# Optimization experiments

Hardware: AMD Instinct MI355X
Metric: run time of the kernel (lower is better)

Reference implementation:

```python
import jax, jax.numpy as jnp
import numpy as np

INPUT, HIDDEN = 128, 64
B, T = 512, 1024


def _lstm_dir(x, Wih, Whh, b):
    """Single-direction LSTM (PyTorch gate order i,f,g,o). x: [B,T,I] -> [B,T,H]."""
    Bn = x.shape[0]
    H = Whh.shape[1]
    # precompute input contributions for all timesteps: [B,T,4H]
    xg = jnp.einsum('bti,gi->btg', x, Wih) + b

    def step(carry, g_t):
        h, c = carry
        g = g_t + h @ Whh.T  # [B,4H]
        i, f, gg, o = jnp.split(g, 4, axis=-1)
        c = jax.nn.sigmoid(f) * c + jax.nn.sigmoid(i) * jnp.tanh(gg)
        h = jax.nn.sigmoid(o) * jnp.tanh(c)
        return (h, c), h

    h0 = jnp.zeros((Bn, H), x.dtype)
    (_, _), hs = jax.lax.scan(step, (h0, h0), jnp.swapaxes(xg, 0, 1))
    return jnp.swapaxes(hs, 0, 1)  # [B,T,H]


def setup_inputs() -> dict:
    key = jax.random.key(0)
    ks = jax.random.split(key, 9)
    s_ih = 1.0 / np.sqrt(HIDDEN)
    def u(k, shape):
        return jax.random.uniform(k, shape, jnp.float32, -s_ih, s_ih)
    return {
        'x': jax.random.normal(ks[0], (B, T, INPUT), jnp.float32),
        'Wih_f': u(ks[1], (4 * HIDDEN, INPUT)),
        'Whh_f': u(ks[2], (4 * HIDDEN, HIDDEN)),
        'b_f': u(ks[3], (4 * HIDDEN,)),   # b_ih + b_hh folded (same math)
        'Wih_b': u(ks[4], (4 * HIDDEN, INPUT)),
        'Whh_b': u(ks[5], (4 * HIDDEN, HIDDEN)),
        'b_b': u(ks[6], (4 * HIDDEN,)),
    }


def reference(x, Wih_f, Whh_f, b_f, Wih_b, Whh_b, b_b):
    # forward returns the full bidirectional sequence output [B,T,2H]
    out_f = _lstm_dir(x, Wih_f, Whh_f, b_f)
    out_b = _lstm_dir(x[:, ::-1], Wih_b, Whh_b, b_b)[:, ::-1]
    return jnp.concatenate([out_f, out_b], axis=-1)
```

## Files before the change

### kernel.cpp

```cpp
#include <hip/hip_runtime.h>

#define T_LEN 1024
#define IN_DIM 128
#define HID 64
#define XSTR 160
#define HSTR 96

typedef __attribute__((ext_vector_type(8))) short short8;
typedef __attribute__((ext_vector_type(4))) float floatx4;
typedef __attribute__((ext_vector_type(2))) float floatx2;

__device__ __forceinline__ unsigned short f2bf(float v) {
    union { float f; unsigned u; } a; a.f = v;
    unsigned r = a.u + 0x7FFFu + ((a.u >> 16) & 1u);
    return (unsigned short)(r >> 16);
}

__device__ __forceinline__ short8 cvt8(const float* p) {
    short8 r;
#pragma unroll
    for (int j = 0; j < 8; ++j) r[j] = (short)f2bf(p[j]);
    return r;
}

#define LOG2E 1.44269504088896f
__device__ __forceinline__ float sigm(float x) {
    return __builtin_amdgcn_rcpf(1.0f + __builtin_amdgcn_exp2f(x * -LOG2E));
}
__device__ __forceinline__ float tanh_(float x) {
    return 2.0f * __builtin_amdgcn_rcpf(1.0f + __builtin_amdgcn_exp2f(x * -2.0f * LOG2E)) - 1.0f;
}


__global__ __launch_bounds__(256, 1) void lstm_bidir(
    const float* __restrict__ x,
    const float* __restrict__ WihF, const float* __restrict__ WhhF, const float* __restrict__ bF,
    const float* __restrict__ WihB, const float* __restrict__ WhhB, const float* __restrict__ bB,
    float* __restrict__ out)
{
    const int tid  = threadIdx.x;
    const int w    = tid >> 6;
    const int lane = tid & 63;
    const int nloc = lane & 15;
    const int quad = lane >> 4;
    const int bid  = blockIdx.x;
    const int dir  = bid & 1;
    const int b0   = (bid >> 1) * 4;

    const float* Wih  = dir ? WihB : WihF;
    const float* Whh  = dir ? WhhB : WhhF;
    const float* bias = dir ? bB   : bF;

    __shared__ unsigned short x_s[2][4 * XSTR];
    __shared__ unsigned short h_s[2][4 * HSTR];

    for (int i = tid; i < 2 * 4 * HSTR; i += 256) ((unsigned short*)h_s)[i] = 0;

    short8 wihf[4][4];
    short8 whhf[4][2];
    float  bv[4];
#pragma unroll
    for (int gc = 0; gc < 4; ++gc) {
        const int row = gc * 64 + w * 16 + nloc;
        bv[gc] = bias[row];
#pragma unroll
        for (int kf = 0; kf < 4; ++kf)
            wihf[gc][kf] = cvt8(Wih + row * IN_DIM + kf * 32 + quad * 8);
#pragma unroll
        for (int kf = 0; kf < 2; ++kf)
            whhf[gc][kf] = cvt8(Whh + row * HID + kf * 32 + quad * 8);
    }

    const int sr = tid >> 6;
    const int sk = (tid & 63) * 2;
    const float* xrow = x + (size_t)(b0 + sr) * T_LEN * IN_DIM + sk;

    auto tmap = [&](int s) {
        int ss = s < T_LEN - 1 ? s : T_LEN - 1;
        return dir ? (T_LEN - 1 - ss) : ss;
    };

    auto stage = [&](int s, int buf) {
        floatx2 v = *(const floatx2*)(xrow + (size_t)tmap(s) * IN_DIM);
        unsigned pack = (unsigned)f2bf(v.x) | ((unsigned)f2bf(v.y) << 16);
        *(unsigned*)&x_s[buf][sr * XSTR + sk] = pack;
    };
    stage(0, 0);
    stage(1, 1);
    floatx2 pfA = *(const floatx2*)(xrow + (size_t)tmap(2) * IN_DIM);
    floatx2 pfB = *(const floatx2*)(xrow + (size_t)tmap(3) * IN_DIM);

    float c = 0.f;

    __syncthreads();

    floatx4 xacc0[4], xacc1[4];
    {
        short8 xa[4];
        const unsigned short* xb = &x_s[0][(nloc >> 2) * XSTR + quad * 8];
#pragma unroll
        for (int kf = 0; kf < 4; ++kf) xa[kf] = *(const short8*)(xb + kf * 32);
        __syncthreads();
#pragma unroll
        for (int gc = 0; gc < 4; ++gc) xacc0[gc] = (floatx4){bv[gc], bv[gc], bv[gc], bv[gc]};
#pragma unroll
        for (int kf = 0; kf < 4; ++kf)
#pragma unroll
            for (int gc = 0; gc < 4; ++gc)
                xacc0[gc] = __builtin_amdgcn_mfma_f32_16x16x32_bf16(xa[kf], wihf[gc][kf], xacc0[gc], 0, 0, 0);
    }

    float* outcol = out + ((size_t)(b0 + quad) * T_LEN) * 128 + dir * HID + w * 16 + nloc;

    auto step = [&](int t, int cur, floatx4* xaccC, floatx4* xaccN, floatx2& pf) {
        floatx2 old = pf;
        pf = *(const floatx2*)(xrow + (size_t)tmap(t + 4) * IN_DIM);

        short8 ha[2];
        const unsigned short* hb = &h_s[cur][(nloc >> 2) * HSTR + quad * 8];
#pragma unroll
        for (int kf = 0; kf < 2; ++kf) ha[kf] = *(const short8*)(hb + kf * 32);

        short8 xa[4];
        const unsigned short* xb = &x_s[cur ^ 1][(nloc >> 2) * XSTR + quad * 8];
#pragma unroll
        for (int kf = 0; kf < 4; ++kf) xa[kf] = *(const short8*)(xb + kf * 32);

        floatx4 acc[4];
#pragma unroll
        for (int gc = 0; gc < 4; ++gc)
            acc[gc] = __builtin_amdgcn_mfma_f32_16x16x32_bf16(ha[0], whhf[gc][0], xaccC[gc], 0, 0, 0);
#pragma unroll
        for (int gc = 0; gc < 4; ++gc)
            acc[gc] = __builtin_amdgcn_mfma_f32_16x16x32_bf16(ha[1], whhf[gc][1], acc[gc], 0, 0, 0);

#pragma unroll
        for (int gc = 0; gc < 4; ++gc) xaccN[gc] = (floatx4){bv[gc], bv[gc], bv[gc], bv[gc]};
#pragma unroll
        for (int kf = 0; kf < 4; ++kf)
#pragma unroll
            for (int gc = 0; gc < 4; ++gc)
                xaccN[gc] = __builtin_amdgcn_mfma_f32_16x16x32_bf16(xa[kf], wihf[gc][kf], xaccN[gc], 0, 0, 0);

        const int tg = tmap(t);
        {
            float iv = sigm(acc[0][0]);
            float fv = sigm(acc[1][0]);
            float gv = tanh_(acc[2][0]);
            float ov = sigm(acc[3][0]);
            c = fv * c + iv * gv;
            float hv = ov * tanh_(c);
            outcol[(size_t)tg * 128] = hv;
            h_s[cur ^ 1][quad * HSTR + w * 16 + nloc] = f2bf(hv);
        }
        {
            unsigned pack = (unsigned)f2bf(old.x) | ((unsigned)f2bf(old.y) << 16);
            *(unsigned*)&x_s[cur][sr * XSTR + sk] = pack;
        }
        __syncthreads();
    };

    for (int t = 0; t < T_LEN; t += 2) {
        step(t,     0, xacc0, xacc1, pfA);
        step(t + 1, 1, xacc1, xacc0, pfB);
    }
}

extern "C" void kernel_launch(void* const* d_in, const int* in_sizes, int n_in,
                              void* d_out, int out_size, void* d_ws, size_t ws_size,
                              hipStream_t stream) {
    const float* x    = (const float*)d_in[0];
    const float* WihF = (const float*)d_in[1];
    const float* WhhF = (const float*)d_in[2];
    const float* bF   = (const float*)d_in[3];
    const float* WihB = (const float*)d_in[4];
    const float* WhhB = (const float*)d_in[5];
    const float* bB   = (const float*)d_in[6];
    float* out = (float*)d_out;

    lstm_bidir<<<dim3(256), dim3(256), 0, stream>>>(x, WihF, WhhF, bF, WihB, WhhB, bB, out);
}
```

Measured before the change: 835.6 us.

## Stage x and output in 8-step chunks through shared memory with vector I/O

Replaces per-timestep scalar x prefetch and scalar output stores with chunked staging: 8 timesteps of x are loaded as float4 per thread one chunk ahead into double-buffered LDS, and h outputs are buffered in LDS and flushed as coalesced float4 stores one chunk later. The aim is to cut global memory transaction count and latency exposure on the serial recurrence path. It adds LDS usage and makes some steps heavier than others (load/convert on the first two steps of each chunk), which can lengthen those iterations.

```diff
diff --git a/kernel.cpp b/kernel.cpp
--- a/kernel.cpp
+++ b/kernel.cpp
@@ -3,12 +3,15 @@
 #define T_LEN 1024
 #define IN_DIM 128
 #define HID 64
+#define CH 8
+#define NCH (T_LEN / CH)
 #define XSTR 160
 #define HSTR 96
+#define OSTR 72
 
 typedef __attribute__((ext_vector_type(8))) short short8;
 typedef __attribute__((ext_vector_type(4))) float floatx4;
-typedef __attribute__((ext_vector_type(2))) float floatx2;
+typedef __attribute__((ext_vector_type(2))) unsigned uintx2;
 
 __device__ __forceinline__ unsigned short f2bf(float v) {
     union { float f; unsigned u; } a; a.f = v;
@@ -30,7 +33,6 @@
 __device__ __forceinline__ float tanh_(float x) {
     return 2.0f * __builtin_amdgcn_rcpf(1.0f + __builtin_amdgcn_exp2f(x * -2.0f * LOG2E)) - 1.0f;
 }
-
 
 __global__ __launch_bounds__(256, 1) void lstm_bidir(
     const float* __restrict__ x,
@@ -51,8 +53,9 @@
     const float* Whh  = dir ? WhhB : WhhF;
     const float* bias = dir ? bB   : bF;
 
-    __shared__ unsigned short x_s[2][4 * XSTR];
-    __shared__ unsigned short h_s[2][4 * HSTR];
+    __shared__ __align__(16) unsigned short xch[2][CH][4 * XSTR];
+    __shared__ __align__(16) unsigned short h_s[2][4 * HSTR];
+    __shared__ __align__(16) float obuf[2][CH][4][OSTR];
 
     for (int i = tid; i < 2 * 4 * HSTR; i += 256) ((unsigned short*)h_s)[i] = 0;
 
@@ -70,25 +73,24 @@
         for (int kf = 0; kf < 2; ++kf)
             whhf[gc][kf] = cvt8(Whh + row * HID + kf * 32 + quad * 8);
     }
-
-    const int sr = tid >> 6;
-    const int sk = (tid & 63) * 2;
-    const float* xrow = x + (size_t)(b0 + sr) * T_LEN * IN_DIM + sk;
 
     auto tmap = [&](int s) {
         int ss = s < T_LEN - 1 ? s : T_LEN - 1;
         return dir ? (T_LEN - 1 - ss) : ss;
     };
 
-    auto stage = [&](int s, int buf) {
-        floatx2 v = *(const floatx2*)(xrow + (size_t)tmap(s) * IN_DIM);
-        unsigned pack = (unsigned)f2bf(v.x) | ((unsigned)f2bf(v.y) << 16);
-        *(unsigned*)&x_s[buf][sr * XSTR + sk] = pack;
-    };
-    stage(0, 0);
-    stage(1, 1);
-    floatx2 pfA = *(const floatx2*)(xrow + (size_t)tmap(2) * IN_DIM);
-    floatx2 pfB = *(const floatx2*)(xrow + (size_t)tmap(3) * IN_DIM);
+    const int g   = tid >> 5;
+    const int l32 = tid & 31;
+
+#pragma unroll
+    for (int i = 0; i < 4; ++i) {
+        floatx4 v = *(const floatx4*)(x + (size_t)(b0 + i) * T_LEN * IN_DIM
+                                        + (size_t)tmap(g) * IN_DIM + l32 * 4);
+        unsigned lo = (unsigned)f2bf(v.x) | ((unsigned)f2bf(v.y) << 16);
+        unsigned hi = (unsigned)f2bf(v.z) | ((unsigned)f2bf(v.w) << 16);
+        uintx2 p = {lo, hi};
+        *(uintx2*)&xch[0][g][i * XSTR + l32 * 4] = p;
+    }
 
     float c = 0.f;
 
@@ -97,10 +99,9 @@
     floatx4 xacc0[4], xacc1[4];
     {
         short8 xa[4];
-        const unsigned short* xb = &x_s[0][(nloc >> 2) * XSTR + quad * 8];
+        const unsigned short* xb = &xch[0][0][(nloc >> 2) * XSTR + quad * 8];
 #pragma unroll
         for (int kf = 0; kf < 4; ++kf) xa[kf] = *(const short8*)(xb + kf * 32);
-        __syncthreads();
 #pragma unroll
         for (int gc = 0; gc < 4; ++gc) xacc0[gc] = (floatx4){bv[gc], bv[gc], bv[gc], bv[gc]};
 #pragma unroll
@@ -110,11 +111,44 @@
                 xacc0[gc] = __builtin_amdgcn_mfma_f32_16x16x32_bf16(xa[kf], wihf[gc][kf], xacc0[gc], 0, 0, 0);
     }
 
-    float* outcol = out + ((size_t)(b0 + quad) * T_LEN) * 128 + dir * HID + w * 16 + nloc;
-
-    auto step = [&](int t, int cur, floatx4* xaccC, floatx4* xaccN, floatx2& pf) {
-        floatx2 old = pf;
-        pf = *(const floatx2*)(xrow + (size_t)tmap(t + 4) * IN_DIM);
+    floatx4 stg[4];
+
+    auto flushPrev = [&](int chkPrev) {
+        const int pb  = chkPrev & 1;
+        const int fs  = tid >> 5;
+        const int fr  = (tid & 31) >> 3;
+        const int fu  = (tid & 7) * 8;
+        const float* src = &obuf[pb][fs][fr][fu];
+        floatx4 v0 = *(const floatx4*)(src);
+        floatx4 v1 = *(const floatx4*)(src + 4);
+        const int tg = tmap(chkPrev * CH + fs);
+        float* dst = out + ((size_t)(b0 + fr) * T_LEN + tg) * 128 + dir * HID + fu;
+        *(floatx4*)(dst)     = v0;
+        *(floatx4*)(dst + 4) = v1;
+    };
+
+    auto step = [&](int sl, int chk, int cbuf, floatx4* xaccC, floatx4* xaccN) {
+        const int cur = sl & 1;
+
+        if (sl == 0) {
+            if (chk > 0) flushPrev(chk - 1);
+            if (chk + 1 < NCH) {
+                const int tn = (chk + 1) * CH + g;
+#pragma unroll
+                for (int i = 0; i < 4; ++i)
+                    stg[i] = *(const floatx4*)(x + (size_t)(b0 + i) * T_LEN * IN_DIM
+                                                 + (size_t)tmap(tn) * IN_DIM + l32 * 4);
+            }
+        }
+        if (sl == 1 && chk + 1 < NCH) {
+#pragma unroll
+            for (int i = 0; i < 4; ++i) {
+                unsigned lo = (unsigned)f2bf(stg[i].x) | ((unsigned)f2bf(stg[i].y) << 16);
+                unsigned hi = (unsigned)f2bf(stg[i].z) | ((unsigned)f2bf(stg[i].w) << 16);
+                uintx2 p = {lo, hi};
+                *(uintx2*)&xch[cbuf ^ 1][g][i * XSTR + l32 * 4] = p;
+            }
+        }
 
         short8 ha[2];
         const unsigned short* hb = &h_s[cur][(nloc >> 2) * HSTR + quad * 8];
@@ -122,7 +156,9 @@
         for (int kf = 0; kf < 2; ++kf) ha[kf] = *(const short8*)(hb + kf * 32);
 
         short8 xa[4];
-        const unsigned short* xb = &x_s[cur ^ 1][(nloc >> 2) * XSTR + quad * 8];
+        const unsigned short* xb = (sl + 1 < CH)
+            ? &xch[cbuf][sl + 1][(nloc >> 2) * XSTR + quad * 8]
+            : &xch[cbuf ^ 1][0][(nloc >> 2) * XSTR + quad * 8];
 #pragma unroll
         for (int kf = 0; kf < 4; ++kf) xa[kf] = *(const short8*)(xb + kf * 32);
 
@@ -142,7 +178,6 @@
             for (int gc = 0; gc < 4; ++gc)
                 xaccN[gc] = __builtin_amdgcn_mfma_f32_16x16x32_bf16(xa[kf], wihf[gc][kf], xaccN[gc], 0, 0, 0);
 
-        const int tg = tmap(t);
         {
             float iv = sigm(acc[0][0]);
             float fv = sigm(acc[1][0]);
@@ -150,20 +185,21 @@
             float ov = sigm(acc[3][0]);
             c = fv * c + iv * gv;
             float hv = ov * tanh_(c);
-            outcol[(size_t)tg * 128] = hv;
+            obuf[cbuf][sl][quad][w * 16 + nloc] = hv;
             h_s[cur ^ 1][quad * HSTR + w * 16 + nloc] = f2bf(hv);
-        }
-        {
-            unsigned pack = (unsigned)f2bf(old.x) | ((unsigned)f2bf(old.y) << 16);
-            *(unsigned*)&x_s[cur][sr * XSTR + sk] = pack;
         }
         __syncthreads();
     };
 
-    for (int t = 0; t < T_LEN; t += 2) {
-        step(t,     0, xacc0, xacc1, pfA);
-        step(t + 1, 1, xacc1, xacc0, pfB);
-    }
+    for (int chk = 0; chk < NCH; ++chk) {
+        const int cbuf = chk & 1;
+#pragma unroll
+        for (int sp = 0; sp < CH; sp += 2) {
+            step(sp,     chk, cbuf, xacc0, xacc1);
+            step(sp + 1, chk, cbuf, xacc1, xacc0);
+        }
+    }
+    flushPrev(NCH - 1);
 }
 
 extern "C" void kernel_launch(void* const* d_in, const int* in_sizes, int n_in,
```

After: 775.1 us. -7.2%, faster.
